# Kernel tuning notes

Measured on AMD Instinct MI355X. Metric: run time of the kernel, lower is better.

The kernel has to match this reference:

```python
import jax, jax.numpy as jnp
import numpy as np

N = 50000       # total nodes
D = 20000       # disease nodes (first D rows)
M = 30000       # mirna nodes
E = 800000      # edges
DSIM = 512; MSIM = 512
HID = 128; OUT = 128; P = 3   # powers p = [0,1,2]
PAIRS = 100000


def _lin(k, o, i):
    s = 1.0 / np.sqrt(i)
    return jax.random.uniform(k, (o, i), jnp.float32, -s, s)


def setup_inputs() -> dict:
    key = jax.random.key(0)
    ks = jax.random.split(key, 24)
    inp = {}
    inp["d_sim"] = jax.random.normal(ks[0], (N, DSIM), jnp.float32)
    inp["m_sim"] = jax.random.normal(ks[1], (N, MSIM), jnp.float32)
    inp["edge_src"] = jax.random.randint(ks[2], (E,), 0, N, jnp.int32)
    inp["edge_dst"] = jax.random.randint(ks[3], (E,), 0, N, jnp.int32)
    inp["src"] = jax.random.randint(ks[4], (PAIRS,), 0, D, jnp.int32)
    inp["dst"] = D + jax.random.randint(ks[5], (PAIRS,), 0, M, jnp.int32)
    # input projections
    inp["d_fc_w"] = _lin(ks[6], HID, DSIM); inp["d_fc_b"] = jnp.zeros((HID,), jnp.float32)
    inp["m_fc_w"] = _lin(ks[7], HID, MSIM); inp["m_fc_b"] = jnp.zeros((HID,), jnp.float32)
    # MixHopConv per-power weights (no bias)
    inp["l0_w"] = jnp.stack([_lin(ks[8 + j], OUT, HID) for j in range(P)])         # [P, OUT, HID]
    inp["l1_w"] = jnp.stack([_lin(ks[11 + j], HID, OUT * P) for j in range(P)])    # [P, HID, OUT*P]
    inp["fc_w"] = _lin(ks[14], OUT, HID * P)
    inp["d_fc1_w"] = _lin(ks[15], OUT, OUT + DSIM); inp["d_fc1_b"] = jnp.zeros((OUT,), jnp.float32)
    inp["m_fc1_w"] = _lin(ks[16], OUT, OUT + MSIM); inp["m_fc1_b"] = jnp.zeros((OUT,), jnp.float32)
    # predictor MLP
    inp["p0_w"] = _lin(ks[17], OUT, 2 * OUT); inp["p0_b"] = jnp.zeros((OUT,), jnp.float32)
    inp["p1_w"] = _lin(ks[18], 1, OUT); inp["p1_b"] = jnp.zeros((1,), jnp.float32)
    return inp


def _mixhop(feats, Ws, edge_src, edge_dst, norm):
    """DGL MixHopConv with p=[0,1,2]: outputs [W_j (D^-1/2 A D^-1/2)^j X for j in p], concatenated."""
    outs = []
    for j in range(P):
        outs.append(feats @ Ws[j].T)
        if j < P - 1:  # propagate one more hop (last hop's propagation is unused)
            feats = feats * norm
            feats = jax.ops.segment_sum(feats[edge_src], edge_dst, num_segments=N)
            feats = feats * norm
    return jnp.concatenate(outs, axis=1)


def reference(d_sim, m_sim, edge_src, edge_dst, src, dst,
              d_fc_w, d_fc_b, m_fc_w, m_fc_b, l0_w, l1_w, fc_w,
              d_fc1_w, d_fc1_b, m_fc1_w, m_fc1_b, p0_w, p0_b, p1_w, p1_b):
    # symmetric normalization from in-degrees (clamped to >= 1)
    degs = jax.ops.segment_sum(jnp.ones((E,), jnp.float32), edge_dst, num_segments=N)
    norm = (jnp.maximum(degs, 1.0) ** -0.5)[:, None]  # [N, 1]
    # per-node-type input projection (dropout = identity in eval)
    z_d = d_sim[:D] @ d_fc_w.T + d_fc_b
    z_m = m_sim[D:] @ m_fc_w.T + m_fc_b
    feats = jnp.concatenate([z_d, z_m], axis=0)               # [N, HID]
    feats = _mixhop(feats, l0_w, edge_src, edge_dst, norm)    # [N, OUT*P]
    feats = _mixhop(feats, l1_w, edge_src, edge_dst, norm)    # [N, HID*P]
    feats = feats @ fc_w.T                                    # [N, OUT]
    h_d = jax.nn.elu(jnp.concatenate([feats[:D], d_sim[:D]], axis=1) @ d_fc1_w.T + d_fc1_b)
    h_m = jax.nn.elu(jnp.concatenate([feats[D:], m_sim[D:]], axis=1) @ m_fc1_w.T + m_fc1_b)
    h = jnp.concatenate([h_d, h_m], axis=0)                   # [N, OUT]
    hc = jnp.concatenate([h[src], h[dst]], axis=1)            # [PAIRS, 2*OUT]
    score = jax.nn.sigmoid(jax.nn.relu(hc @ p0_w.T + p0_b) @ p1_w.T + p1_b)
    return score
```

## Files before the change

kernel.cpp:

```cpp
#include <hip/hip_runtime.h>
#include <cstddef>
#include <cstdint>

#define N_NODES 50000
#define D_NODES 20000
#define M_NODES 30000
#define E_EDGES 800000
#define PAIRS_N 100000

typedef unsigned short u16;
typedef unsigned int u32;
typedef short bf16x8 __attribute__((ext_vector_type(8)));
typedef float f32x4 __attribute__((ext_vector_type(4)));

__device__ __forceinline__ float bf2f(u16 u) {
  u32 v = ((u32)u) << 16;
  return __builtin_bit_cast(float, v);
}
__device__ __forceinline__ u16 f2bf(float f) {
  u32 u = __builtin_bit_cast(u32, f);
  u32 r = (u + 0x7fffu + ((u >> 16) & 1u)) >> 16;
  return (u16)r;
}
__device__ __forceinline__ u32 pk2(float x, float y) {
  return (u32)f2bf(x) | ((u32)f2bf(y) << 16);
}

__global__ void wconv_kernel(const float* s0, const float* s1, const float* s2,
                             const float* s3, const float* s4,
                             u16* d0, u16* d1, u16* d2, u16* d3, u16* d4) {
  int i = blockIdx.x * 256 + threadIdx.x;
  const float* s; u16* d; int l;
  if      (i < 16384) { s = s0; d = d0; l = i; }
  else if (i < 32768) { s = s1; d = d1; l = i - 16384; }
  else if (i < 53248) { s = s2; d = d2; l = i - 32768; }
  else if (i < 73728) { s = s3; d = d3; l = i - 53248; }
  else if (i < 81920) { s = s4; d = d4; l = i - 73728; }
  else return;
  float4 v = *(const float4*)(s + (size_t)l * 4);
  ushort4 o;
  o.x = f2bf(v.x); o.y = f2bf(v.y); o.z = f2bf(v.z); o.w = f2bf(v.w);
  *(ushort4*)(d + (size_t)l * 4) = o;
}

__global__ void wcomb1_kernel(const float* __restrict__ l1w, const float* __restrict__ l0w,
                              float* __restrict__ Tmp) {
  int pj = blockIdx.x;
  int p = pj / 3, j = pj % 3;
  int o = blockIdx.y;
  int i = threadIdx.x;
  const float* wp = l1w + (size_t)p * 49152 + (size_t)o * 384 + 128 * j;
  const float* wj = l0w + (size_t)j * 16384 + i;
  float acc = 0.f;
#pragma unroll 4
  for (int t = 0; t < 128; ++t) acc += wp[t] * wj[(size_t)t * 128];
  Tmp[(size_t)pj * 16384 + (size_t)o * 128 + i] = acc;
}
__global__ void wcomb2_kernel(const float* __restrict__ fcw, const float* __restrict__ Tmp,
                              u16* __restrict__ G) {
  int k = blockIdx.x;
  int of = blockIdx.y;
  int i = threadIdx.x;
  float acc = 0.f;
  int plo = (k > 2) ? (k - 2) : 0;
  int phi = (k < 2) ? k : 2;
  for (int p = plo; p <= phi; ++p) {
    int j = k - p;
    const float* fp = fcw + (size_t)of * 384 + 128 * p;
    const float* tp = Tmp + (size_t)(p * 3 + j) * 16384 + i;
#pragma unroll 4
    for (int t = 0; t < 128; ++t) acc += fp[t] * tp[(size_t)t * 128];
  }
  G[(size_t)of * 640 + 128 * k + i] = f2bf(acc);
}

__global__ void deg_count_kernel(const int* __restrict__ dst, int* __restrict__ degs, int e) {
  int i = blockIdx.x * 256 + threadIdx.x;
  if (i < e) atomicAdd(&degs[dst[i]], 1);
}
__global__ void norm_reduce_kernel(const int* __restrict__ degs, float* __restrict__ norm,
                                   int n, int* __restrict__ bsums) {
  __shared__ int s[256];
  int t = threadIdx.x;
  int i = blockIdx.x * 256 + t;
  int d = (i < n) ? degs[i] : 0;
  if (i < n) norm[i] = rsqrtf(fmaxf((float)d, 1.0f));
  s[t] = d;
  __syncthreads();
  for (int st = 128; st > 0; st >>= 1) {
    if (t < st) s[t] += s[t + st];
    __syncthreads();
  }
  if (t == 0) bsums[blockIdx.x] = s[0];
}
__global__ void scan_small_kernel(int* b, int nb) {
  __shared__ int s[256];
  int t = threadIdx.x;
  int orig = (t < nb) ? b[t] : 0;
  s[t] = orig;
  __syncthreads();
  for (int st = 1; st < 256; st <<= 1) {
    int v = (t >= st) ? s[t - st] : 0;
    __syncthreads();
    s[t] += v;
    __syncthreads();
  }
  if (t < nb) b[t] = s[t] - orig;
}
__global__ void scan_final_kernel(const int* __restrict__ degs, const int* __restrict__ boff,
                                  int* __restrict__ out, int* __restrict__ cursor,
                                  int n, int total) {
  __shared__ int s[256];
  int t = threadIdx.x;
  int i = blockIdx.x * 256 + t;
  int orig = (i < n) ? degs[i] : 0;
  s[t] = orig;
  __syncthreads();
  for (int st = 1; st < 256; st <<= 1) {
    int v = (t >= st) ? s[t - st] : 0;
    __syncthreads();
    s[t] += v;
    __syncthreads();
  }
  if (i < n) {
    int v = boff[blockIdx.x] + s[t] - orig;
    out[i] = v;
    cursor[i] = v;
  }
  if (i == 0) out[n] = total;
}
__global__ void fill_csr_kernel(const int* __restrict__ esrc, const int* __restrict__ edst,
                                int* __restrict__ cursor, int* __restrict__ csr_src, int e) {
  int i = blockIdx.x * 256 + threadIdx.x;
  if (i < e) {
    int p = atomicAdd(&cursor[edst[i]], 1);
    csr_src[p] = esrc[i];
  }
}

__global__ void prop128_kernel(const u16* __restrict__ in,
                               u16* __restrict__ outu, int ldu, int cOff,
                               u16* __restrict__ outs,
                               const int* __restrict__ off, const int* __restrict__ srcs,
                               const float* __restrict__ norm) {
  __shared__ float red[4][128];
  const int node = blockIdx.x;
  const int tid = threadIdx.x;
  const int g = tid >> 5, lane = tid & 31;
  const int e0 = off[node], e1 = off[node + 1];
  const int cnt = e1 - e0;
  const int lo = e0 + ((cnt * g) >> 2);
  const int hi = e0 + ((cnt * (g + 1)) >> 2);
  float a0 = 0.f, a1 = 0.f, a2 = 0.f, a3 = 0.f;
  const u16* basec = in + (lane << 2);
  for (int base = lo; base < hi; base += 32) {
    int nE = hi - base; if (nE > 32) nE = 32;
    int myE = srcs[base + ((lane < nE) ? lane : (nE - 1))];
#pragma unroll 4
    for (int i = 0; i < nE; ++i) {
      int s = __builtin_amdgcn_readlane(myE, i);
      uint2 v = *(const uint2*)(basec + ((size_t)s << 7));
      a0 += bf2f((u16)v.x); a1 += bf2f((u16)(v.x >> 16));
      a2 += bf2f((u16)v.y); a3 += bf2f((u16)(v.y >> 16));
    }
  }
  float* rg = red[g];
  rg[(lane << 2) + 0] = a0; rg[(lane << 2) + 1] = a1;
  rg[(lane << 2) + 2] = a2; rg[(lane << 2) + 3] = a3;
  __syncthreads();
  if (tid < 64) {
    int c0 = tid << 1;
    float s0 = red[0][c0] + red[1][c0] + red[2][c0] + red[3][c0];
    float s1 = red[0][c0 + 1] + red[1][c0 + 1] + red[2][c0 + 1] + red[3][c0 + 1];
    float nd = norm[node];
    *(u32*)(outu + (size_t)node * ldu + cOff + c0) = pk2(s0 * nd, s1 * nd);
    if (outs) {
      float nd2 = nd * nd;
      *(u32*)(outs + ((size_t)node << 7) + c0) = pk2(s0 * nd2, s1 * nd2);
    }
  }
}

__global__ __launch_bounds__(256) void mfma_gemm_kernel(
    const void* __restrict__ A1a, const void* __restrict__ A1b, int lda1, int K1, int a1f32,
    const void* __restrict__ A2a, const void* __restrict__ A2b, int lda2, int K2, int a2f32,
    const int* __restrict__ gsrc, const int* __restrict__ gdst,
    const u16* __restrict__ Wa, const u16* __restrict__ Wb,
    const float* __restrict__ biasa, const float* __restrict__ biasb,
    int splitB, int rowD, int boundA, int nrows,
    u16* __restrict__ Cu, int ldcu, int colOff,
    u16* __restrict__ Cs, const float* __restrict__ normp,
    int act) {
  __shared__ u32 As[64 * 32];
  __shared__ u32 Ws[128 * 32];
  const int tid = threadIdx.x;
  const bool segb = (int)blockIdx.x >= splitB;
  const int brow = segb ? rowD + ((int)blockIdx.x - splitB) * 64 : (int)blockIdx.x * 64;
  const int bound = segb ? nrows : boundA;
  const void* A1 = segb ? A1b : A1a;
  const void* A2 = segb ? A2b : A2a;
  const u16* W = segb ? Wb : Wa;
  const float* bias = segb ? biasb : biasa;
  const int K = K1 + K2;
  const int lane = tid & 63;
  const int wv = tid >> 6;
  const int wr = (wv >> 1) * 32;
  const int wc = (wv & 1) * 64;
  const int fr = lane & 15;
  const int fg = lane >> 4;

  f32x4 acc[2][4];
#pragma unroll
  for (int m = 0; m < 2; ++m)
#pragma unroll
    for (int n = 0; n < 4; ++n) acc[m][n] = (f32x4){0.f, 0.f, 0.f, 0.f};

  const int sr = tid >> 2, sk = tid & 3;
  const int swc = tid >> 1, sh = tid & 1;
  const int prow = (brow + sr < bound) ? (brow + sr) : (bound - 1);

  for (int kc = 0; kc < K; kc += 64) {
    uint4 qa0, qa1;
    {
      bool seg1 = kc < K1;
      int kk = seg1 ? kc : kc - K1;
      const void* Av = seg1 ? A1 : A2;
      int ld = seg1 ? lda1 : lda2;
      int isf = seg1 ? a1f32 : a2f32;
      int row = gsrc ? (seg1 ? gsrc[prow] : gdst[prow]) : prow;
      if (isf) {
        const float* p = (const float*)Av + (size_t)row * ld + kk + sk * 16;
        float4 f0 = ((const float4*)p)[0];
        float4 f1 = ((const float4*)p)[1];
        float4 f2 = ((const float4*)p)[2];
        float4 f3 = ((const float4*)p)[3];
        qa0 = make_uint4(pk2(f0.x, f0.y), pk2(f0.z, f0.w), pk2(f1.x, f1.y), pk2(f1.z, f1.w));
        qa1 = make_uint4(pk2(f2.x, f2.y), pk2(f2.z, f2.w), pk2(f3.x, f3.y), pk2(f3.z, f3.w));
      } else {
        const u16* p = (const u16*)Av + (size_t)row * ld + kk + sk * 16;
        qa0 = *(const uint4*)p;
        qa1 = *(const uint4*)(p + 8);
      }
    }
    const u16* wp = W + (size_t)swc * K + kc + sh * 32;
    uint4 qw0 = *(const uint4*)(wp);
    uint4 qw1 = *(const uint4*)(wp + 8);
    uint4 qw2 = *(const uint4*)(wp + 16);
    uint4 qw3 = *(const uint4*)(wp + 24);

    __syncthreads();
    *(uint4*)&As[sr * 32 + ((2 * sk)     ^ (sr & 7)) * 4] = qa0;
    *(uint4*)&As[sr * 32 + ((2 * sk + 1) ^ (sr & 7)) * 4] = qa1;
    *(uint4*)&Ws[swc * 32 + ((sh * 4 + 0) ^ (swc & 7)) * 4] = qw0;
    *(uint4*)&Ws[swc * 32 + ((sh * 4 + 1) ^ (swc & 7)) * 4] = qw1;
    *(uint4*)&Ws[swc * 32 + ((sh * 4 + 2) ^ (swc & 7)) * 4] = qw2;
    *(uint4*)&Ws[swc * 32 + ((sh * 4 + 3) ^ (swc & 7)) * 4] = qw3;
    __syncthreads();

#pragma unroll
    for (int kk2 = 0; kk2 < 2; ++kk2) {
      int gix = kk2 * 4 + fg;
      int r0 = wr + fr, r1 = wr + 16 + fr;
      bf16x8 aF0 = *(const bf16x8*)&As[r0 * 32 + (gix ^ (r0 & 7)) * 4];
      bf16x8 aF1 = *(const bf16x8*)&As[r1 * 32 + (gix ^ (r1 & 7)) * 4];
#pragma unroll
      for (int n = 0; n < 4; ++n) {
        int cr = wc + n * 16 + fr;
        bf16x8 bF = *(const bf16x8*)&Ws[cr * 32 + (gix ^ (cr & 7)) * 4];
        acc[0][n] = __builtin_amdgcn_mfma_f32_16x16x32_bf16(aF0, bF, acc[0][n], 0, 0, 0);
        acc[1][n] = __builtin_amdgcn_mfma_f32_16x16x32_bf16(aF1, bF, acc[1][n], 0, 0, 0);
      }
    }
  }

#pragma unroll
  for (int m = 0; m < 2; ++m) {
#pragma unroll
    for (int n = 0; n < 4; ++n) {
      int ccol = wc + n * 16 + fr;
      float b = bias ? bias[ccol] : 0.f;
#pragma unroll
      for (int i = 0; i < 4; ++i) {
        int row = brow + wr + m * 16 + (lane >> 4) * 4 + i;
        if (row < bound) {
          float v = acc[m][n][i] + b;
          if (act == 1) v = (v > 0.f) ? v : (expf(v) - 1.f);
          else if (act == 2) v = fmaxf(v, 0.f);
          Cu[(size_t)row * ldcu + colOff + ccol] = f2bf(v);
          if (Cs) Cs[((size_t)row << 7) + ccol] = f2bf(v * normp[row]);
        }
      }
    }
  }
}

__global__ void score_kernel(const u16* __restrict__ hidden, const float* __restrict__ p1w,
                             const float* __restrict__ p1b, float* __restrict__ out, int pairs) {
  int pr = blockIdx.x * 4 + (threadIdx.x >> 6);
  int lane = threadIdx.x & 63;
  if (pr >= pairs) return;
  const u16* h = hidden + (size_t)pr * 128;
  float v = bf2f(h[lane]) * p1w[lane] + bf2f(h[lane + 64]) * p1w[lane + 64];
  for (int off = 32; off > 0; off >>= 1) v += __shfl_down(v, off);
  if (lane == 0) out[pr] = 1.f / (1.f + expf(-(v + p1b[0])));
}

extern "C" void kernel_launch(void* const* d_in, const int* in_sizes, int n_in,
                              void* d_out, int out_size, void* d_ws, size_t ws_size,
                              hipStream_t stream) {
  const float* d_sim   = (const float*)d_in[0];
  const float* m_sim   = (const float*)d_in[1];
  const int*   e_src   = (const int*)d_in[2];
  const int*   e_dst   = (const int*)d_in[3];
  const int*   p_src   = (const int*)d_in[4];
  const int*   p_dst   = (const int*)d_in[5];
  const float* d_fc_w  = (const float*)d_in[6];
  const float* d_fc_b  = (const float*)d_in[7];
  const float* m_fc_w  = (const float*)d_in[8];
  const float* m_fc_b  = (const float*)d_in[9];
  const float* l0_w    = (const float*)d_in[10];
  const float* l1_w    = (const float*)d_in[11];
  const float* fc_w    = (const float*)d_in[12];
  const float* d_fc1_w = (const float*)d_in[13];
  const float* d_fc1_b = (const float*)d_in[14];
  const float* m_fc1_w = (const float*)d_in[15];
  const float* m_fc1_b = (const float*)d_in[16];
  const float* p0_w    = (const float*)d_in[17];
  const float* p0_b    = (const float*)d_in[18];
  const float* p1_w    = (const float*)d_in[19];
  const float* p1_b    = (const float*)d_in[20];
  float* out = (float*)d_out;

  const int N = N_NODES, D = D_NODES, M = M_NODES, E = E_EDGES, NP = PAIRS_N;

  u16* ws16 = (u16*)d_ws;
  u16* HCAT = ws16;
  u16* HSa  = HCAT + (size_t)N * 640;
  u16* HSb  = HSa + (size_t)N * 128;
  u16* FE   = HSb + (size_t)N * 128;
  u16* HB   = FE  + (size_t)N * 128;
  u16* HID  = HB  + (size_t)N * 128;
  u16* wb_dfc  = HID + (size_t)NP * 128;
  u16* wb_mfc  = wb_dfc  + 65536;
  u16* wb_dfc1 = wb_mfc  + 65536;
  u16* wb_mfc1 = wb_dfc1 + 81920;
  u16* wb_p0   = wb_mfc1 + 81920;
  u16* wb_G    = wb_p0   + 32768;
  u16* wend    = wb_G    + 81920;
  size_t off16 = (size_t)(wend - ws16);
  off16 = (off16 + 1) & ~(size_t)1;
  float* Tmp   = (float*)(ws16 + off16);
  float* normp = Tmp + 9 * 16384;
  int* degs    = (int*)(normp + N);
  int* csr_off = degs + N;
  int* cursor  = csr_off + N + 1;
  int* csr_src = cursor + N;
  int* bsums   = csr_src + E;

  const int nb = (N + 255) / 256;
  const int eb = (E + 255) / 256;

  wconv_kernel<<<320, 256, 0, stream>>>(d_fc_w, m_fc_w, d_fc1_w, m_fc1_w, p0_w,
                                        wb_dfc, wb_mfc, wb_dfc1, wb_mfc1, wb_p0);
  wcomb1_kernel<<<dim3(9, 128), 128, 0, stream>>>(l1_w, l0_w, Tmp);
  wcomb2_kernel<<<dim3(5, 128), 128, 0, stream>>>(fc_w, Tmp, wb_G);

  hipMemsetAsync(degs, 0, (size_t)N * 4, stream);
  deg_count_kernel<<<eb, 256, 0, stream>>>(e_dst, degs, E);
  norm_reduce_kernel<<<nb, 256, 0, stream>>>(degs, normp, N, bsums);
  scan_small_kernel<<<1, 256, 0, stream>>>(bsums, nb);
  scan_final_kernel<<<nb, 256, 0, stream>>>(degs, bsums, csr_off, cursor, N, E);
  fill_csr_kernel<<<eb, 256, 0, stream>>>(e_src, e_dst, cursor, csr_src, E);

  const int GDseg = (D + 63) / 64;
  const int GMseg = (M + 63) / 64;
  const int GSEG = GDseg + GMseg;
  const int GN = (N + 63) / 64, GP = (NP + 63) / 64;

  mfma_gemm_kernel<<<GSEG, 256, 0, stream>>>(
      d_sim, m_sim, 512, 512, 1, nullptr, nullptr, 0, 0, 0, nullptr, nullptr,
      wb_dfc, wb_mfc, d_fc_b, m_fc_b, GDseg, D, D, N,
      HCAT, 640, 0, HSa, normp, 0);

  prop128_kernel<<<N, 128, 0, stream>>>(HSa, HCAT, 640, 128, HSb, csr_off, csr_src, normp);
  prop128_kernel<<<N, 128, 0, stream>>>(HSb, HCAT, 640, 256, HSa, csr_off, csr_src, normp);
  prop128_kernel<<<N, 128, 0, stream>>>(HSa, HCAT, 640, 384, HSb, csr_off, csr_src, normp);
  prop128_kernel<<<N, 128, 0, stream>>>(HSb, HCAT, 640, 512, nullptr, csr_off, csr_src, normp);

  mfma_gemm_kernel<<<GN, 256, 0, stream>>>(
      HCAT, HCAT, 640, 640, 0, nullptr, nullptr, 0, 0, 0, nullptr, nullptr,
      wb_G, wb_G, nullptr, nullptr, GN, 0, N, N,
      FE, 128, 0, nullptr, normp, 0);

  mfma_gemm_kernel<<<GSEG, 256, 0, stream>>>(
      FE, FE, 128, 128, 0, d_sim, m_sim, 512, 512, 1, nullptr, nullptr,
      wb_dfc1, wb_mfc1, d_fc1_b, m_fc1_b, GDseg, D, D, N,
      HB, 128, 0, nullptr, normp, 1);

  mfma_gemm_kernel<<<GP, 256, 0, stream>>>(
      HB, HB, 128, 128, 0, HB, HB, 128, 128, 0, p_src, p_dst,
      wb_p0, wb_p0, p0_b, p0_b, GP, 0, NP, NP,
      HID, 128, 0, nullptr, normp, 2);

  score_kernel<<<(NP + 3) / 4, 256, 0, stream>>>(HID, p1_w, p1_b, out, NP);

  (void)in_sizes; (void)n_in; (void)out_size; (void)ws_size;
}
```

Measured before the change: 434.0 us.

## Use wave-per-node propagation, 32-row GEMM tiles, and fuse score into predictor GEMM

The propagation kernel now assigns one 64-lane wave per node instead of a 128-thread block split four ways. This drops the shared-memory reduction and barrier and unrolls the gather by eight to keep more loads in flight. The GEMM tile shrinks from 64 to 32 rows to launch more blocks. The final p1 dot product and sigmoid are fused into the predictor GEMM epilogue, which removes the hidden buffer write/read and the separate score kernel. The risks are less per-node parallelism for high-degree nodes and lower MFMA reuse per block.

```diff
diff --git a/kernel.cpp b/kernel.cpp
--- a/kernel.cpp
+++ b/kernel.cpp
@@ -138,46 +138,58 @@
   }
 }
 
-__global__ void prop128_kernel(const u16* __restrict__ in,
-                               u16* __restrict__ outu, int ldu, int cOff,
-                               u16* __restrict__ outs,
-                               const int* __restrict__ off, const int* __restrict__ srcs,
-                               const float* __restrict__ norm) {
-  __shared__ float red[4][128];
-  const int node = blockIdx.x;
-  const int tid = threadIdx.x;
-  const int g = tid >> 5, lane = tid & 31;
+__global__ void prop_kernel(const u16* __restrict__ in,
+                            u16* __restrict__ outu, int ldu, int cOff,
+                            u16* __restrict__ outs,
+                            const int* __restrict__ off, const int* __restrict__ srcs,
+                            const float* __restrict__ norm, int nnodes) {
+  const int node = blockIdx.x * 4 + (threadIdx.x >> 6);
+  if (node >= nnodes) return;
+  const int lane = threadIdx.x & 63;
   const int e0 = off[node], e1 = off[node + 1];
-  const int cnt = e1 - e0;
-  const int lo = e0 + ((cnt * g) >> 2);
-  const int hi = e0 + ((cnt * (g + 1)) >> 2);
-  float a0 = 0.f, a1 = 0.f, a2 = 0.f, a3 = 0.f;
-  const u16* basec = in + (lane << 2);
-  for (int base = lo; base < hi; base += 32) {
-    int nE = hi - base; if (nE > 32) nE = 32;
+  float a0 = 0.f, a1 = 0.f;
+  const u16* basec = in + (lane << 1);
+  for (int base = e0; base < e1; base += 64) {
+    int nE = e1 - base; if (nE > 64) nE = 64;
     int myE = srcs[base + ((lane < nE) ? lane : (nE - 1))];
-#pragma unroll 4
-    for (int i = 0; i < nE; ++i) {
+    int i = 0;
+    for (; i + 8 <= nE; i += 8) {
+      int s0 = __builtin_amdgcn_readlane(myE, i + 0);
+      int s1 = __builtin_amdgcn_readlane(myE, i + 1);
+      int s2 = __builtin_amdgcn_readlane(myE, i + 2);
+      int s3 = __builtin_amdgcn_readlane(myE, i + 3);
+      int s4 = __builtin_amdgcn_readlane(myE, i + 4);
+      int s5 = __builtin_amdgcn_readlane(myE, i + 5);
+      int s6 = __builtin_amdgcn_readlane(myE, i + 6);
+      int s7 = __builtin_amdgcn_readlane(myE, i + 7);
+      u32 v0 = *(const u32*)(basec + ((size_t)s0 << 7));
+      u32 v1 = *(const u32*)(basec + ((size_t)s1 << 7));
+      u32 v2 = *(const u32*)(basec + ((size_t)s2 << 7));
+      u32 v3 = *(const u32*)(basec + ((size_t)s3 << 7));
+      u32 v4 = *(const u32*)(basec + ((size_t)s4 << 7));
+      u32 v5 = *(const u32*)(basec + ((size_t)s5 << 7));
+      u32 v6 = *(const u32*)(basec + ((size_t)s6 << 7));
+      u32 v7 = *(const u32*)(basec + ((size_t)s7 << 7));
+      a0 += bf2f((u16)v0); a1 += bf2f((u16)(v0 >> 16));
+      a0 += bf2f((u16)v1); a1 += bf2f((u16)(v1 >> 16));
+      a0 += bf2f((u16)v2); a1 += bf2f((u16)(v2 >> 16));
+      a0 += bf2f((u16)v3); a1 += bf2f((u16)(v3 >> 16));
+      a0 += bf2f((u16)v4); a1 += bf2f((u16)(v4 >> 16));
+      a0 += bf2f((u16)v5); a1 += bf2f((u16)(v5 >> 16));
+      a0 += bf2f((u16)v6); a1 += bf2f((u16)(v6 >> 16));
+      a0 += bf2f((u16)v7); a1 += bf2f((u16)(v7 >> 16));
+    }
+    for (; i < nE; ++i) {
       int s = __builtin_amdgcn_readlane(myE, i);
-      uint2 v = *(const uint2*)(basec + ((size_t)s << 7));
-      a0 += bf2f((u16)v.x); a1 += bf2f((u16)(v.x >> 16));
-      a2 += bf2f((u16)v.y); a3 += bf2f((u16)(v.y >> 16));
-    }
-  }
-  float* rg = red[g];
-  rg[(lane << 2) + 0] = a0; rg[(lane << 2) + 1] = a1;
-  rg[(lane << 2) + 2] = a2; rg[(lane << 2) + 3] = a3;
-  __syncthreads();
-  if (tid < 64) {
-    int c0 = tid << 1;
-    float s0 = red[0][c0] + red[1][c0] + red[2][c0] + red[3][c0];
-    float s1 = red[0][c0 + 1] + red[1][c0 + 1] + red[2][c0 + 1] + red[3][c0 + 1];
-    float nd = norm[node];
-    *(u32*)(outu + (size_t)node * ldu + cOff + c0) = pk2(s0 * nd, s1 * nd);
-    if (outs) {
-      float nd2 = nd * nd;
-      *(u32*)(outs + ((size_t)node << 7) + c0) = pk2(s0 * nd2, s1 * nd2);
-    }
+      u32 v = *(const u32*)(basec + ((size_t)s << 7));
+      a0 += bf2f((u16)v); a1 += bf2f((u16)(v >> 16));
+    }
+  }
+  float nd = norm[node];
+  *(u32*)(outu + (size_t)node * ldu + cOff + (lane << 1)) = pk2(a0 * nd, a1 * nd);
+  if (outs) {
+    float nd2 = nd * nd;
+    *(u32*)(outs + ((size_t)node << 7) + (lane << 1)) = pk2(a0 * nd2, a1 * nd2);
   }
 }
 
@@ -190,12 +202,13 @@
     int splitB, int rowD, int boundA, int nrows,
     u16* __restrict__ Cu, int ldcu, int colOff,
     u16* __restrict__ Cs, const float* __restrict__ normp,
+    const float* __restrict__ p1w, const float* __restrict__ p1b, float* __restrict__ outf,
     int act) {
-  __shared__ u32 As[64 * 32];
+  __shared__ u32 As[32 * 32];
   __shared__ u32 Ws[128 * 32];
   const int tid = threadIdx.x;
   const bool segb = (int)blockIdx.x >= splitB;
-  const int brow = segb ? rowD + ((int)blockIdx.x - splitB) * 64 : (int)blockIdx.x * 64;
+  const int brow = segb ? rowD + ((int)blockIdx.x - splitB) * 32 : (int)blockIdx.x * 32;
   const int bound = segb ? nrows : boundA;
   const void* A1 = segb ? A1b : A1a;
   const void* A2 = segb ? A2b : A2a;
@@ -204,42 +217,35 @@
   const int K = K1 + K2;
   const int lane = tid & 63;
   const int wv = tid >> 6;
-  const int wr = (wv >> 1) * 32;
-  const int wc = (wv & 1) * 64;
   const int fr = lane & 15;
   const int fg = lane >> 4;
 
-  f32x4 acc[2][4];
+  f32x4 acc[2][2];
 #pragma unroll
   for (int m = 0; m < 2; ++m)
 #pragma unroll
-    for (int n = 0; n < 4; ++n) acc[m][n] = (f32x4){0.f, 0.f, 0.f, 0.f};
-
-  const int sr = tid >> 2, sk = tid & 3;
+    for (int n = 0; n < 2; ++n) acc[m][n] = (f32x4){0.f, 0.f, 0.f, 0.f};
+
+  const int sr = tid >> 3, sk = tid & 7;
   const int swc = tid >> 1, sh = tid & 1;
   const int prow = (brow + sr < bound) ? (brow + sr) : (bound - 1);
 
   for (int kc = 0; kc < K; kc += 64) {
-    uint4 qa0, qa1;
+    uint4 qa;
     {
       bool seg1 = kc < K1;
-      int kk = seg1 ? kc : kc - K1;
+      int kk = (seg1 ? kc : kc - K1) + sk * 8;
       const void* Av = seg1 ? A1 : A2;
       int ld = seg1 ? lda1 : lda2;
       int isf = seg1 ? a1f32 : a2f32;
       int row = gsrc ? (seg1 ? gsrc[prow] : gdst[prow]) : prow;
       if (isf) {
-        const float* p = (const float*)Av + (size_t)row * ld + kk + sk * 16;
+        const float* p = (const float*)Av + (size_t)row * ld + kk;
         float4 f0 = ((const float4*)p)[0];
         float4 f1 = ((const float4*)p)[1];
-        float4 f2 = ((const float4*)p)[2];
-        float4 f3 = ((const float4*)p)[3];
-        qa0 = make_uint4(pk2(f0.x, f0.y), pk2(f0.z, f0.w), pk2(f1.x, f1.y), pk2(f1.z, f1.w));
-        qa1 = make_uint4(pk2(f2.x, f2.y), pk2(f2.z, f2.w), pk2(f3.x, f3.y), pk2(f3.z, f3.w));
+        qa = make_uint4(pk2(f0.x, f0.y), pk2(f0.z, f0.w), pk2(f1.x, f1.y), pk2(f1.z, f1.w));
       } else {
-        const u16* p = (const u16*)Av + (size_t)row * ld + kk + sk * 16;
-        qa0 = *(const uint4*)p;
-        qa1 = *(const uint4*)(p + 8);
+        qa = *(const uint4*)((const u16*)Av + (size_t)row * ld + kk);
       }
     }
     const u16* wp = W + (size_t)swc * K + kc + sh * 32;
@@ -249,8 +255,7 @@
     uint4 qw3 = *(const uint4*)(wp + 24);
 
     __syncthreads();
-    *(uint4*)&As[sr * 32 + ((2 * sk)     ^ (sr & 7)) * 4] = qa0;
-    *(uint4*)&As[sr * 32 + ((2 * sk + 1) ^ (sr & 7)) * 4] = qa1;
+    *(uint4*)&As[sr * 32 + (sk ^ (sr & 7)) * 4] = qa;
     *(uint4*)&Ws[swc * 32 + ((sh * 4 + 0) ^ (swc & 7)) * 4] = qw0;
     *(uint4*)&Ws[swc * 32 + ((sh * 4 + 1) ^ (swc & 7)) * 4] = qw1;
     *(uint4*)&Ws[swc * 32 + ((sh * 4 + 2) ^ (swc & 7)) * 4] = qw2;
@@ -260,12 +265,12 @@
 #pragma unroll
     for (int kk2 = 0; kk2 < 2; ++kk2) {
       int gix = kk2 * 4 + fg;
-      int r0 = wr + fr, r1 = wr + 16 + fr;
+      int r0 = fr, r1 = 16 + fr;
       bf16x8 aF0 = *(const bf16x8*)&As[r0 * 32 + (gix ^ (r0 & 7)) * 4];
       bf16x8 aF1 = *(const bf16x8*)&As[r1 * 32 + (gix ^ (r1 & 7)) * 4];
 #pragma unroll
-      for (int n = 0; n < 4; ++n) {
-        int cr = wc + n * 16 + fr;
+      for (int n = 0; n < 2; ++n) {
+        int cr = wv * 32 + n * 16 + fr;
         bf16x8 bF = *(const bf16x8*)&Ws[cr * 32 + (gix ^ (cr & 7)) * 4];
         acc[0][n] = __builtin_amdgcn_mfma_f32_16x16x32_bf16(aF0, bF, acc[0][n], 0, 0, 0);
         acc[1][n] = __builtin_amdgcn_mfma_f32_16x16x32_bf16(aF1, bF, acc[1][n], 0, 0, 0);
@@ -273,15 +278,60 @@
     }
   }
 
+  if (act == 3) {
+    float part[2][4];
+#pragma unroll
+    for (int m = 0; m < 2; ++m)
+#pragma unroll
+      for (int i = 0; i < 4; ++i) part[m][i] = 0.f;
+#pragma unroll
+    for (int n = 0; n < 2; ++n) {
+      int ccol = wv * 32 + n * 16 + fr;
+      float b = bias[ccol];
+      float pw = p1w[ccol];
+#pragma unroll
+      for (int m = 0; m < 2; ++m)
+#pragma unroll
+        for (int i = 0; i < 4; ++i) {
+          float v = acc[m][n][i] + b;
+          v = fmaxf(v, 0.f);
+          part[m][i] += v * pw;
+        }
+    }
+#pragma unroll
+    for (int mask = 1; mask <= 8; mask <<= 1)
+#pragma unroll
+      for (int m = 0; m < 2; ++m)
+#pragma unroll
+        for (int i = 0; i < 4; ++i) part[m][i] += __shfl_xor(part[m][i], mask);
+    __syncthreads();
+    float* sred = (float*)As;
+    if (fr == 0) {
+#pragma unroll
+      for (int m = 0; m < 2; ++m)
+#pragma unroll
+        for (int i = 0; i < 4; ++i) sred[wv * 32 + m * 16 + fg * 4 + i] = part[m][i];
+    }
+    __syncthreads();
+    if (tid < 32) {
+      int row = brow + tid;
+      if (row < bound) {
+        float s = sred[tid] + sred[32 + tid] + sred[64 + tid] + sred[96 + tid] + p1b[0];
+        outf[row] = 1.f / (1.f + expf(-s));
+      }
+    }
+    return;
+  }
+
 #pragma unroll
   for (int m = 0; m < 2; ++m) {
 #pragma unroll
-    for (int n = 0; n < 4; ++n) {
-      int ccol = wc + n * 16 + fr;
+    for (int n = 0; n < 2; ++n) {
+      int ccol = wv * 32 + n * 16 + fr;
       float b = bias ? bias[ccol] : 0.f;
 #pragma unroll
       for (int i = 0; i < 4; ++i) {
-        int row = brow + wr + m * 16 + (lane >> 4) * 4 + i;
+        int row = brow + m * 16 + fg * 4 + i;
         if (row < bound) {
           float v = acc[m][n][i] + b;
           if (act == 1) v = (v > 0.f) ? v : (expf(v) - 1.f);
@@ -292,17 +342,6 @@
       }
     }
   }
-}
-
-__global__ void score_kernel(const u16* __restrict__ hidden, const float* __restrict__ p1w,
-                             const float* __restrict__ p1b, float* __restrict__ out, int pairs) {
-  int pr = blockIdx.x * 4 + (threadIdx.x >> 6);
-  int lane = threadIdx.x & 63;
-  if (pr >= pairs) return;
-  const u16* h = hidden + (size_t)pr * 128;
-  float v = bf2f(h[lane]) * p1w[lane] + bf2f(h[lane + 64]) * p1w[lane + 64];
-  for (int off = 32; off > 0; off >>= 1) v += __shfl_down(v, off);
-  if (lane == 0) out[pr] = 1.f / (1.f + expf(-(v + p1b[0])));
 }
 
 extern "C" void kernel_launch(void* const* d_in, const int* in_sizes, int n_in,
@@ -339,8 +378,7 @@
   u16* HSb  = HSa + (size_t)N * 128;
   u16* FE   = HSb + (size_t)N * 128;
   u16* HB   = FE  + (size_t)N * 128;
-  u16* HID  = HB  + (size_t)N * 128;
-  u16* wb_dfc  = HID + (size_t)NP * 128;
+  u16* wb_dfc  = HB + (size_t)N * 128;
   u16* wb_mfc  = wb_dfc  + 65536;
   u16* wb_dfc1 = wb_mfc  + 65536;
   u16* wb_mfc1 = wb_dfc1 + 81920;
@@ -372,37 +410,37 @@
   scan_final_kernel<<<nb, 256, 0, stream>>>(degs, bsums, csr_off, cursor, N, E);
   fill_csr_kernel<<<eb, 256, 0, stream>>>(e_src, e_dst, cursor, csr_src, E);
 
-  const int GDseg = (D + 63) / 64;
-  const int GMseg = (M + 63) / 64;
+  const int GDseg = D / 32;
+  const int GMseg = (M + 31) / 32;
   const int GSEG = GDseg + GMseg;
-  const int GN = (N + 63) / 64, GP = (NP + 63) / 64;
+  const int GN = (N + 31) / 32;
+  const int GP = (NP + 31) / 32;
+  const int GPROP = (N + 3) / 4;
 
   mfma_gemm_kernel<<<GSEG, 256, 0, stream>>>(
       d_sim, m_sim, 512, 512, 1, nullptr, nullptr, 0, 0, 0, nullptr, nullptr,
       wb_dfc, wb_mfc, d_fc_b, m_fc_b, GDseg, D, D, N,
-      HCAT, 640, 0, HSa, normp, 0);
-
-  prop128_kernel<<<N, 128, 0, stream>>>(HSa, HCAT, 640, 128, HSb, csr_off, csr_src, normp);
-  prop128_kernel<<<N, 128, 0, stream>>>(HSb, HCAT, 640, 256, HSa, csr_off, csr_src, normp);
-  prop128_kernel<<<N, 128, 0, stream>>>(HSa, HCAT, 640, 384, HSb, csr_off, csr_src, normp);
-  prop128_kernel<<<N, 128, 0, stream>>>(HSb, HCAT, 640, 512, nullptr, csr_off, csr_src, normp);
+      HCAT, 640, 0, HSa, normp, nullptr, nullptr, nullptr, 0);
+
+  prop_kernel<<<GPROP, 256, 0, stream>>>(HSa, HCAT, 640, 128, HSb, csr_off, csr_src, normp, N);
+  prop_kernel<<<GPROP, 256, 0, stream>>>(HSb, HCAT, 640, 256, HSa, csr_off, csr_src, normp, N);
+  prop_kernel<<<GPROP, 256, 0, stream>>>(HSa, HCAT, 640, 384, HSb, csr_off, csr_src, normp, N);
+  prop_kernel<<<GPROP, 256, 0, stream>>>(HSb, HCAT, 640, 512, nullptr, csr_off, csr_src, normp, N);
 
   mfma_gemm_kernel<<<GN, 256, 0, stream>>>(
       HCAT, HCAT, 640, 640, 0, nullptr, nullptr, 0, 0, 0, nullptr, nullptr,
       wb_G, wb_G, nullptr, nullptr, GN, 0, N, N,
-      FE, 128, 0, nullptr, normp, 0);
+      FE, 128, 0, nullptr, normp, nullptr, nullptr, nullptr, 0);
 
   mfma_gemm_kernel<<<GSEG, 256, 0, stream>>>(
       FE, FE, 128, 128, 0, d_sim, m_sim, 512, 512, 1, nullptr, nullptr,
       wb_dfc1, wb_mfc1, d_fc1_b, m_fc1_b, GDseg, D, D, N,
-      HB, 128, 0, nullptr, normp, 1);
+      HB, 128, 0, nullptr, normp, nullptr, nullptr, nullptr, 1);
 
   mfma_gemm_kernel<<<GP, 256, 0, stream>>>(
       HB, HB, 128, 128, 0, HB, HB, 128, 128, 0, p_src, p_dst,
       wb_p0, wb_p0, p0_b, p0_b, GP, 0, NP, NP,
-      HID, 128, 0, nullptr, normp, 2);
-
-  score_kernel<<<(NP + 3) / 4, 256, 0, stream>>>(HID, p1_w, p1_b, out, NP);
+      nullptr, 128, 0, nullptr, normp, p1_w, p1_b, out, 3);
 
   (void)in_sizes; (void)n_in; (void)out_size; (void)ws_size;
 }
```

New measurement: 379.1 us. -12.7%, faster.
